# Optimization experiments

Measured on AMD Instinct MI355X. Metric: run time of the kernel, lower is better.

## Reference

```python
import jax, jax.numpy as jnp
import numpy as np

PAD = 0
C_CONST = 0.1712209


def setup_inputs() -> dict:
    key = jax.random.key(0)
    ks = jax.random.split(key, 6)
    tlen, bsz, slen, hsize, vocab = 64, 32, 64, 1024, 32000
    hidden = jax.random.normal(ks[0], (tlen, bsz, hsize), dtype=jnp.float32)
    context = jax.random.normal(ks[1], (slen, bsz, hsize), dtype=jnp.float32)
    src = jax.random.randint(ks[2], (bsz, slen), 0, vocab, dtype=jnp.int64)
    stdv = 1.0 / np.sqrt(hsize)
    W_gen = jax.random.uniform(ks[3], (vocab, hsize), dtype=jnp.float32, minval=-stdv, maxval=stdv)
    b_gen = jnp.zeros((vocab,), dtype=jnp.float32)
    # Xavier-like init for the copy gate
    w_copy = jax.random.normal(ks[4], (hsize,), dtype=jnp.float32) * np.sqrt(2.0 / (hsize + 1))
    b_copy = jnp.zeros((1,), dtype=jnp.float32)
    return {"hidden": hidden, "context": context, "src": src,
            "W_gen": W_gen, "b_gen": b_gen, "w_copy": w_copy, "b_copy": b_copy}


def reference(hidden, context, src, W_gen, b_gen, w_copy, b_copy):
    tlen, bsz, hsize = hidden.shape
    # p(z=1): probability of copying, [tlen, bsz, 1]
    copy_prob = jax.nn.sigmoid(jnp.einsum('tbh,h->tb', hidden, w_copy) + b_copy[0])[..., None]
    # generator distribution over tgt vocab
    logits = jnp.einsum('tbh,vh->tbv', hidden, W_gen) + b_gen
    prob = jax.nn.softmax(logits.astype(jnp.float32), axis=-1)
    p_g = prob * (1.0 - copy_prob)  # [tlen, bsz, vocab]
    # copy attention over source positions: bmm(query[b,t,h], keys[b,s,h]^T)
    attn_score = jnp.einsum('tbh,sbh->bts', hidden, context)  # [bsz, tlen, slen]
    src_mask = (src == PAD)[:, None, :]  # [bsz, 1, slen]
    attn_score = jnp.where(src_mask, -jnp.inf, attn_score.astype(jnp.float32))
    attns = jax.nn.softmax(attn_score, axis=-1)  # [bsz, tlen, slen]
    p_c = jnp.transpose(attns, (1, 0, 2)) * copy_prob  # [tlen, bsz, slen]
    # scatter_add copy probs into vocab distribution along dim 2
    slen = src.shape[1]
    idx_src = jnp.broadcast_to(src[None, :, :], (tlen, bsz, slen))
    t_idx = jnp.arange(tlen)[:, None, None]
    b_idx = jnp.arange(bsz)[None, :, None]
    p_g = p_g.at[t_idx, b_idx, idx_src].add(p_c)
    return jnp.log(p_g) + C_CONST
```

## Files before the change

### kernel.cpp

```cpp
#include <hip/hip_runtime.h>
#include <hip/hip_bf16.h>
#include <stdint.h>

#define TLEN 64
#define BSZ 32
#define SLEN 64
#define HS 1024
#define VOC 32000
#define NROW (TLEN*BSZ)
#define C_CONST_F 0.1712209f

typedef __attribute__((ext_vector_type(8))) short short8;
typedef __attribute__((ext_vector_type(4))) float f32x4;

static __device__ __forceinline__ ushort f2bf(float f) {
    uint32_t u = __builtin_bit_cast(uint32_t, f);
    uint32_t r = (u + 0x7fffu + ((u >> 16) & 1u)) >> 16;
    return (ushort)r;
}

static __device__ __forceinline__ void async16(const void* g, void* lds) {
    __builtin_amdgcn_global_load_lds(
        (const __attribute__((address_space(1))) void*)g,
        (__attribute__((address_space(3))) void*)lds, 16, 0, 0);
}

__global__ __launch_bounds__(256) void gate_kernel(const float* __restrict__ hidden,
                                                   const float* __restrict__ w_copy,
                                                   const float* __restrict__ b_copy,
                                                   float* __restrict__ cp) {
    int wid = threadIdx.x >> 6, lane = threadIdx.x & 63;
    int row = blockIdx.x * 4 + wid;
    const float* h = hidden + (size_t)row * HS;
    float acc = 0.f;
    for (int i = 0; i < 4; ++i) {
        int off = (i * 64 + lane) * 4;
        float4 a = *(const float4*)(h + off);
        float4 w = *(const float4*)(w_copy + off);
        acc += a.x * w.x + a.y * w.y + a.z * w.z + a.w * w.w;
    }
    for (int m = 32; m >= 1; m >>= 1) acc += __shfl_xor(acc, m, 64);
    if (lane == 0) cp[row] = 1.f / (1.f + expf(-(acc + b_copy[0])));
}

__global__ __launch_bounds__(256) void attn_kernel(const float* __restrict__ hidden,
                                                   const float* __restrict__ context,
                                                   const int* __restrict__ src,
                                                   const float* __restrict__ cp,
                                                   float* __restrict__ p_c) {
    int row = blockIdx.x;
    int b = row & (BSZ - 1);
    int tid = threadIdx.x, wid = tid >> 6, lane = tid & 63;
    __shared__ float hrow[HS];
    __shared__ float sc[SLEN];
    *(float4*)(hrow + tid * 4) = *(const float4*)(hidden + (size_t)row * HS + tid * 4);
    __syncthreads();
    for (int j = 0; j < 16; ++j) {
        int s = wid * 16 + j;
        const float* c = context + ((size_t)s * BSZ + b) * HS;
        float acc = 0.f;
        for (int i = 0; i < 4; ++i) {
            int off = (i * 64 + lane) * 4;
            float4 cv = *(const float4*)(c + off);
            float4 hv = *(const float4*)(hrow + off);
            acc += cv.x * hv.x + cv.y * hv.y + cv.z * hv.z + cv.w * hv.w;
        }
        for (int m = 32; m >= 1; m >>= 1) acc += __shfl_xor(acc, m, 64);
        if (lane == 0) sc[s] = acc;
    }
    __syncthreads();
    if (tid < SLEN) {
        float v = sc[tid];
        if (src[b * SLEN + tid] == 0) v = -INFINITY;
        float m = v;
        for (int k = 32; k >= 1; k >>= 1) m = fmaxf(m, __shfl_xor(m, k, 64));
        float e = expf(v - m);
        float ssum = e;
        for (int k = 32; k >= 1; k >>= 1) ssum += __shfl_xor(ssum, k, 64);
        p_c[row * SLEN + tid] = (e / ssum) * cp[row];
    }
}

__global__ __launch_bounds__(256) void cvt_kernel(const float* __restrict__ in,
                                                  ushort* __restrict__ out, int n4) {
    int i = blockIdx.x * blockDim.x + threadIdx.x;
    if (i >= n4) return;
    float4 v = ((const float4*)in)[i];
    ushort4 o;
    o.x = f2bf(v.x); o.y = f2bf(v.y); o.z = f2bf(v.z); o.w = f2bf(v.w);
    ((ushort4*)out)[i] = o;
}

__global__ __launch_bounds__(256) void gemm_kernel(const ushort* __restrict__ A,
                                                   const ushort* __restrict__ B,
                                                   const float* __restrict__ b_gen,
                                                   float* __restrict__ out,
                                                   float* __restrict__ partials ) {
    __shared__ ushort sA[128 * 32];
    __shared__ ushort sB[128 * 32];
    int bid = blockIdx.x;
    int mIdx = bid & 15;
    int nIdx = bid >> 4;
    int m0 = mIdx * 128, n0 = nIdx * 128;
    int tid = threadIdx.x, wid = tid >> 6, lane = tid & 63;
    int wm = (wid >> 1) * 64, wn = (wid & 1) * 64;
    int lr = lane & 15, lg = lane >> 4;

    f32x4 acc[4][4];
    for (int m = 0; m < 4; ++m)
        for (int n = 0; n < 4; ++n)
            acc[m][n] = f32x4{0.f, 0.f, 0.f, 0.f};

    for (int k0 = 0; k0 < HS; k0 += 32) {
        for (int rep = 0; rep < 2; ++rep) {
            int i = tid + 256 * rep;
            int r = i >> 2, c = (i & 3) * 8;
            const ushort* ga = A + (size_t)(m0 + r) * HS + k0 + c;
            const ushort* gb = B + (size_t)(n0 + r) * HS + k0 + c;
            char* la = (char*)sA + (size_t)(wid * 64 + 256 * rep) * 16;
            char* lb = (char*)sB + (size_t)(wid * 64 + 256 * rep) * 16;
            async16(ga, la);
            async16(gb, lb);
        }
        __syncthreads();
        short8 af[4], bf[4];
        for (int mb = 0; mb < 4; ++mb)
            af[mb] = *(const short8*)(sA + (wm + mb * 16 + lr) * 32 + lg * 8);
        for (int nb = 0; nb < 4; ++nb)
            bf[nb] = *(const short8*)(sB + (wn + nb * 16 + lr) * 32 + lg * 8);
        for (int mb = 0; mb < 4; ++mb)
            for (int nb = 0; nb < 4; ++nb)
                acc[mb][nb] = __builtin_amdgcn_mfma_f32_16x16x32_bf16(af[mb], bf[nb], acc[mb][nb], 0, 0, 0);
        __syncthreads();
    }

    float bg[4];
    for (int nb = 0; nb < 4; ++nb) bg[nb] = b_gen[n0 + wn + nb * 16 + lr];
    int chunk = nIdx * 2 + (wid & 1);
    for (int mb = 0; mb < 4; ++mb) {
        for (int r = 0; r < 4; ++r) {
            int row = m0 + wm + mb * 16 + lg * 4 + r;
            float v[4];
            float mx = -INFINITY;
            for (int nb = 0; nb < 4; ++nb) {
                v[nb] = acc[mb][nb][r] + bg[nb];
                mx = fmaxf(mx, v[nb]);
                out[(size_t)row * VOC + n0 + wn + nb * 16 + lr] = v[nb];
            }
            for (int k = 8; k >= 1; k >>= 1) mx = fmaxf(mx, __shfl_xor(mx, k, 16));
            float se = 0.f;
            for (int nb = 0; nb < 4; ++nb) se += __expf(v[nb] - mx);
            for (int k = 8; k >= 1; k >>= 1) se += __shfl_xor(se, k, 16);
            if (lr == 0) {
                float2 pv; pv.x = mx; pv.y = se;
                *(float2*)(partials + ((size_t)row * 500 + chunk) * 2) = pv;
            }
        }
    }
}

__global__ __launch_bounds__(256) void reduce_kernel(const float* __restrict__ partials,
                                                     float* __restrict__ Ms,
                                                     float* __restrict__ Ss) {
    int wid = threadIdx.x >> 6, lane = threadIdx.x & 63;
    int row = blockIdx.x * 4 + wid;
    float m = -INFINITY, s = 0.f;
    for (int c = lane; c < 500; c += 64) {
        float2 p = *(const float2*)(partials + ((size_t)row * 500 + c) * 2);
        float nm = fmaxf(m, p.x);
        s = s * __expf(m - nm) + p.y * __expf(p.x - nm);
        m = nm;
    }
    for (int k = 32; k >= 1; k >>= 1) {
        float om = __shfl_xor(m, k, 64), os = __shfl_xor(s, k, 64);
        float nm = fmaxf(m, om);
        s = s * __expf(m - nm) + os * __expf(om - nm);
        m = nm;
    }
    if (lane == 0) { Ms[row] = m; Ss[row] = s; }
}

__global__ __launch_bounds__(256) void finalize_kernel(const int* __restrict__ src,
                                                       const float* __restrict__ p_c,
                                                       const float* __restrict__ cp,
                                                       const float* __restrict__ Ms,
                                                       const float* __restrict__ Ss,
                                                       float* __restrict__ out) {
    int row = blockIdx.y;
    int c0 = blockIdx.x * 1280;
    int b = row & (BSZ - 1);
    __shared__ float addv[1280];
    int tid = threadIdx.x;
    for (int i = tid; i < 1280; i += 256) addv[i] = 0.f;
    __syncthreads();
    if (tid < SLEN) {
        int v = src[b * SLEN + tid];
        if (v >= c0 && v < c0 + 1280) {
            atomicAdd(&addv[v - c0], p_c[row * SLEN + tid]);
        }
    }
    __syncthreads();
    float M = Ms[row];
    float g = (1.f - cp[row]) / Ss[row];
    size_t base = (size_t)row * VOC;
    for (int i = 0; i < 5; ++i) {
        int col = c0 + i * 256 + tid;
        float L = out[base + col];
        float p = __expf(L - M) * g + addv[i * 256 + tid];
        out[base + col] = __logf(p) + C_CONST_F;
    }
}

extern "C" void kernel_launch(void* const* d_in, const int* in_sizes, int n_in,
                              void* d_out, int out_size, void* d_ws, size_t ws_size,
                              hipStream_t stream) {
    const float* hidden  = (const float*)d_in[0];
    const float* context = (const float*)d_in[1];
    const int*   src     = (const int*)d_in[2];
    const float* W_gen   = (const float*)d_in[3];
    const float* b_gen   = (const float*)d_in[4];
    const float* w_copy  = (const float*)d_in[5];
    const float* b_copy  = (const float*)d_in[6];
    float* out = (float*)d_out;
    char* ws = (char*)d_ws;

    float*  cp       = (float*)(ws);
    float*  p_c      = (float*)(ws + 8192);
    float*  Ms       = (float*)(ws + 532480);
    float*  Ss       = (float*)(ws + 540672);
    float*  partials = (float*)(ws + 548864);
    ushort* Abf      = (ushort*)(ws + 8740864);
    ushort* Wbf      = (ushort*)(ws + 12935168);

    gate_kernel<<<NROW / 4, 256, 0, stream>>>(hidden, w_copy, b_copy, cp);
    attn_kernel<<<NROW, 256, 0, stream>>>(hidden, context, src, cp, p_c);
    cvt_kernel<<<(NROW * HS / 4) / 256, 256, 0, stream>>>(hidden, Abf, NROW * HS / 4);
    cvt_kernel<<<(VOC * HS / 4) / 256, 256, 0, stream>>>(W_gen, Wbf, VOC * HS / 4);
    gemm_kernel<<<(NROW / 128) * (VOC / 128), 256, 0, stream>>>(Abf, Wbf, b_gen, out, partials);
    reduce_kernel<<<NROW / 4, 256, 0, stream>>>(partials, Ms, Ss);
    dim3 fgrid(VOC / 1280, NROW);
    finalize_kernel<<<fgrid, 256, 0, stream>>>(src, p_c, cp, Ms, Ss, out);
}
```

Before: 389.8 us.

## Store GEMM logits as bf16, deepen K tile with swizzled LDS, vectorize finalize

The GEMM K-step goes from 32 to 64 and uses an XOR-swizzled LDS layout so fragment reads avoid bank conflicts. Workgroup order is remapped so neighbouring blocks share tiles of the large B matrix. When the workspace is big enough, logits are staged through LDS and written as bf16 to a scratch buffer, which roughly halves the intermediate write and read traffic. Finalize processes 16 contiguous columns per thread with vector loads and stores. The bf16 logits lose precision before the exp/log step, and there is a fallback path that keeps fp32 logits.

```diff
diff --git a/kernel.cpp b/kernel.cpp
--- a/kernel.cpp
+++ b/kernel.cpp
@@ -9,6 +9,7 @@
 #define VOC 32000
 #define NROW (TLEN*BSZ)
 #define C_CONST_F 0.1712209f
+#define BK 64
 
 typedef __attribute__((ext_vector_type(8))) short short8;
 typedef __attribute__((ext_vector_type(4))) float f32x4;
@@ -18,12 +19,16 @@
     uint32_t r = (u + 0x7fffu + ((u >> 16) & 1u)) >> 16;
     return (ushort)r;
 }
-
+static __device__ __forceinline__ float bf2f(ushort u) {
+    uint32_t v = ((uint32_t)u) << 16;
+    return __builtin_bit_cast(float, v);
+}
 static __device__ __forceinline__ void async16(const void* g, void* lds) {
     __builtin_amdgcn_global_load_lds(
         (const __attribute__((address_space(1))) void*)g,
         (__attribute__((address_space(3))) void*)lds, 16, 0, 0);
 }
+static __device__ __forceinline__ int swz12(int e) { return e ^ (((e >> 4) & 15) << 1); }
 
 __global__ __launch_bounds__(256) void gate_kernel(const float* __restrict__ hidden,
                                                    const float* __restrict__ w_copy,
@@ -91,61 +96,97 @@
     ((ushort4*)out)[i] = o;
 }
 
+template <bool BF16L>
 __global__ __launch_bounds__(256) void gemm_kernel(const ushort* __restrict__ A,
                                                    const ushort* __restrict__ B,
                                                    const float* __restrict__ b_gen,
-                                                   float* __restrict__ out,
+                                                   void* __restrict__ logits,
                                                    float* __restrict__ partials ) {
-    __shared__ ushort sA[128 * 32];
-    __shared__ ushort sB[128 * 32];
-    int bid = blockIdx.x;
-    int mIdx = bid & 15;
-    int nIdx = bid >> 4;
+    __shared__ ushort sAB[2 * 128 * BK];
+    ushort* sA = sAB;
+    ushort* sB = sAB + 128 * BK;
+
+    int orig = blockIdx.x;
+    int wg = (orig & 7) * 500 + (orig >> 3);
+    int mIdx = wg & 15;
+    int nIdx = wg >> 4;
     int m0 = mIdx * 128, n0 = nIdx * 128;
     int tid = threadIdx.x, wid = tid >> 6, lane = tid & 63;
     int wm = (wid >> 1) * 64, wn = (wid & 1) * 64;
     int lr = lane & 15, lg = lane >> 4;
 
+    const ushort* gaP[4]; const ushort* gbP[4]; char* laP[4]; char* lbP[4];
+    for (int j = 0; j < 4; ++j) {
+        int slot = j * 256 + tid;
+        int row = slot >> 3;
+        int cc = (slot & 7) ^ (row & 7);
+        gaP[j] = A + (size_t)(m0 + row) * HS + cc * 8;
+        gbP[j] = B + (size_t)(n0 + row) * HS + cc * 8;
+        laP[j] = (char*)sA + (size_t)(j * 256 + wid * 64) * 16;
+        lbP[j] = (char*)sB + (size_t)(j * 256 + wid * 64) * 16;
+    }
+
     f32x4 acc[4][4];
     for (int m = 0; m < 4; ++m)
         for (int n = 0; n < 4; ++n)
             acc[m][n] = f32x4{0.f, 0.f, 0.f, 0.f};
 
-    for (int k0 = 0; k0 < HS; k0 += 32) {
-        for (int rep = 0; rep < 2; ++rep) {
-            int i = tid + 256 * rep;
-            int r = i >> 2, c = (i & 3) * 8;
-            const ushort* ga = A + (size_t)(m0 + r) * HS + k0 + c;
-            const ushort* gb = B + (size_t)(n0 + r) * HS + k0 + c;
-            char* la = (char*)sA + (size_t)(wid * 64 + 256 * rep) * 16;
-            char* lb = (char*)sB + (size_t)(wid * 64 + 256 * rep) * 16;
-            async16(ga, la);
-            async16(gb, lb);
+    int offA[4][2], offB[4][2];
+    for (int mb = 0; mb < 4; ++mb) {
+        int row = wm + mb * 16 + lr;
+        for (int kk = 0; kk < 2; ++kk)
+            offA[mb][kk] = row * (BK * 2) + (((kk * 4 + lg) ^ (row & 7)) << 4);
+    }
+    for (int nb = 0; nb < 4; ++nb) {
+        int row = wn + nb * 16 + lr;
+        for (int kk = 0; kk < 2; ++kk)
+            offB[nb][kk] = row * (BK * 2) + (((kk * 4 + lg) ^ (row & 7)) << 4);
+    }
+
+    for (int k0 = 0; k0 < HS; k0 += BK) {
+        for (int j = 0; j < 4; ++j) {
+            async16(gaP[j] + k0, laP[j]);
+            async16(gbP[j] + k0, lbP[j]);
         }
         __syncthreads();
-        short8 af[4], bf[4];
-        for (int mb = 0; mb < 4; ++mb)
-            af[mb] = *(const short8*)(sA + (wm + mb * 16 + lr) * 32 + lg * 8);
-        for (int nb = 0; nb < 4; ++nb)
-            bf[nb] = *(const short8*)(sB + (wn + nb * 16 + lr) * 32 + lg * 8);
-        for (int mb = 0; mb < 4; ++mb)
+        for (int kk = 0; kk < 2; ++kk) {
+            short8 af[4], bfr[4];
+            for (int mb = 0; mb < 4; ++mb)
+                af[mb] = *(const short8*)((const char*)sA + offA[mb][kk]);
             for (int nb = 0; nb < 4; ++nb)
-                acc[mb][nb] = __builtin_amdgcn_mfma_f32_16x16x32_bf16(af[mb], bf[nb], acc[mb][nb], 0, 0, 0);
+                bfr[nb] = *(const short8*)((const char*)sB + offB[nb][kk]);
+            for (int mb = 0; mb < 4; ++mb)
+                for (int nb = 0; nb < 4; ++nb)
+                    acc[mb][nb] = __builtin_amdgcn_mfma_f32_16x16x32_bf16(af[mb], bfr[nb], acc[mb][nb], 0, 0, 0);
+        }
         __syncthreads();
     }
 
     float bg[4];
     for (int nb = 0; nb < 4; ++nb) bg[nb] = b_gen[n0 + wn + nb * 16 + lr];
     int chunk = nIdx * 2 + (wid & 1);
+    ushort* stile = sAB + wid * 4096;
+
     for (int mb = 0; mb < 4; ++mb) {
         for (int r = 0; r < 4; ++r) {
-            int row = m0 + wm + mb * 16 + lg * 4 + r;
+            int rl = mb * 16 + lg * 4 + r;
+            int row = m0 + wm + rl;
             float v[4];
             float mx = -INFINITY;
             for (int nb = 0; nb < 4; ++nb) {
                 v[nb] = acc[mb][nb][r] + bg[nb];
                 mx = fmaxf(mx, v[nb]);
-                out[(size_t)row * VOC + n0 + wn + nb * 16 + lr] = v[nb];
+            }
+            if (BF16L) {
+                for (int nb = 0; nb < 4; ++nb) {
+                    int cl = nb * 16 + lr;
+                    int slot_w = (cl >> 3) ^ (rl & 7);
+                    stile[rl * 64 + slot_w * 8 + (cl & 7)] = f2bf(v[nb]);
+                }
+            } else {
+                float* out = (float*)logits;
+                for (int nb = 0; nb < 4; ++nb)
+                    out[(size_t)row * VOC + n0 + wn + nb * 16 + lr] = v[nb];
             }
             for (int k = 8; k >= 1; k >>= 1) mx = fmaxf(mx, __shfl_xor(mx, k, 16));
             float se = 0.f;
@@ -155,6 +196,17 @@
                 float2 pv; pv.x = mx; pv.y = se;
                 *(float2*)(partials + ((size_t)row * 500 + chunk) * 2) = pv;
             }
+        }
+    }
+    if (BF16L) {
+        __syncthreads();
+        ushort* Lbf = (ushort*)logits;
+        for (int rep = 0; rep < 8; ++rep) {
+            int rl = rep * 8 + (lane >> 3);
+            int slot_r = (lane & 7) ^ (rl & 7);
+            short8 val = *(const short8*)(stile + rl * 64 + slot_r * 8);
+            ushort* dst = Lbf + (size_t)(m0 + wm + rl) * VOC + n0 + wn + (lane & 7) * 8;
+            *(short8*)dst = val;
         }
     }
 }
@@ -180,34 +232,54 @@
     if (lane == 0) { Ms[row] = m; Ss[row] = s; }
 }
 
+template <bool BF16L>
 __global__ __launch_bounds__(256) void finalize_kernel(const int* __restrict__ src,
                                                        const float* __restrict__ p_c,
                                                        const float* __restrict__ cp,
                                                        const float* __restrict__ Ms,
                                                        const float* __restrict__ Ss,
+                                                       const void* __restrict__ logits,
                                                        float* __restrict__ out) {
     int row = blockIdx.y;
-    int c0 = blockIdx.x * 1280;
+    int c0 = blockIdx.x * 4096;
     int b = row & (BSZ - 1);
-    __shared__ float addv[1280];
+    __shared__ float addv[4096];
     int tid = threadIdx.x;
-    for (int i = tid; i < 1280; i += 256) addv[i] = 0.f;
+    for (int i = tid; i < 4096; i += 256) addv[i] = 0.f;
     __syncthreads();
     if (tid < SLEN) {
         int v = src[b * SLEN + tid];
-        if (v >= c0 && v < c0 + 1280) {
-            atomicAdd(&addv[v - c0], p_c[row * SLEN + tid]);
-        }
+        if (v >= c0 && v < c0 + 4096)
+            atomicAdd(&addv[swz12(v - c0)], p_c[row * SLEN + tid]);
     }
     __syncthreads();
+    int col = c0 + tid * 16;
+    if (col >= VOC) return;
     float M = Ms[row];
     float g = (1.f - cp[row]) / Ss[row];
-    size_t base = (size_t)row * VOC;
-    for (int i = 0; i < 5; ++i) {
-        int col = c0 + i * 256 + tid;
-        float L = out[base + col];
-        float p = __expf(L - M) * g + addv[i * 256 + tid];
-        out[base + col] = __logf(p) + C_CONST_F;
+    float L[16];
+    if (BF16L) {
+        const ushort* lb = (const ushort*)logits + (size_t)row * VOC + col;
+        short8 a = *(const short8*)lb;
+        short8 c = *(const short8*)(lb + 8);
+        for (int i = 0; i < 8; ++i) { L[i] = bf2f((ushort)a[i]); L[8 + i] = bf2f((ushort)c[i]); }
+    } else {
+        const float* lf = (const float*)logits + (size_t)row * VOC + col;
+        for (int i = 0; i < 4; ++i) {
+            float4 v = *(const float4*)(lf + i * 4);
+            L[i * 4 + 0] = v.x; L[i * 4 + 1] = v.y; L[i * 4 + 2] = v.z; L[i * 4 + 3] = v.w;
+        }
+    }
+    float res[16];
+    for (int i = 0; i < 16; ++i) {
+        float p = __expf(L[i] - M) * g + addv[swz12(tid * 16 + i)];
+        res[i] = __logf(p) + C_CONST_F;
+    }
+    float* op = out + (size_t)row * VOC + col;
+    for (int i = 0; i < 4; ++i) {
+        float4 v;
+        v.x = res[i * 4 + 0]; v.y = res[i * 4 + 1]; v.z = res[i * 4 + 2]; v.w = res[i * 4 + 3];
+        *(float4*)(op + i * 4) = v;
     }
 }
 
@@ -231,13 +303,22 @@
     float*  partials = (float*)(ws + 548864);
     ushort* Abf      = (ushort*)(ws + 8740864);
     ushort* Wbf      = (ushort*)(ws + 12935168);
+    ushort* Lbf      = (ushort*)(ws + 78471168);
+    const size_t NEED_BF16 = 209543168;
 
     gate_kernel<<<NROW / 4, 256, 0, stream>>>(hidden, w_copy, b_copy, cp);
     attn_kernel<<<NROW, 256, 0, stream>>>(hidden, context, src, cp, p_c);
     cvt_kernel<<<(NROW * HS / 4) / 256, 256, 0, stream>>>(hidden, Abf, NROW * HS / 4);
     cvt_kernel<<<(VOC * HS / 4) / 256, 256, 0, stream>>>(W_gen, Wbf, VOC * HS / 4);
-    gemm_kernel<<<(NROW / 128) * (VOC / 128), 256, 0, stream>>>(Abf, Wbf, b_gen, out, partials);
-    reduce_kernel<<<NROW / 4, 256, 0, stream>>>(partials, Ms, Ss);
-    dim3 fgrid(VOC / 1280, NROW);
-    finalize_kernel<<<fgrid, 256, 0, stream>>>(src, p_c, cp, Ms, Ss, out);
-}
+
+    dim3 fgrid(8, NROW);
+    if (ws_size >= NEED_BF16) {
+        gemm_kernel<true><<<(NROW / 128) * (VOC / 128), 256, 0, stream>>>(Abf, Wbf, b_gen, Lbf, partials);
+        reduce_kernel<<<NROW / 4, 256, 0, stream>>>(partials, Ms, Ss);
+        finalize_kernel<true><<<fgrid, 256, 0, stream>>>(src, p_c, cp, Ms, Ss, Lbf, out);
+    } else {
+        gemm_kernel<false><<<(NROW / 128) * (VOC / 128), 256, 0, stream>>>(Abf, Wbf, b_gen, out, partials);
+        reduce_kernel<<<NROW / 4, 256, 0, stream>>>(partials, Ms, Ss);
+        finalize_kernel<false><<<fgrid, 256, 0, stream>>>(src, p_c, cp, Ms, Ss, out, out);
+    }
+}
```

Result: no change. 391.9 us (+0.6%).
